# Kernel tuning notes

Measured on AMD Instinct MI355X. Metric: run time of the kernel, lower is better.

The kernel has to match this reference:

```python
import jax, jax.numpy as jnp
import numpy as np

B, N, D_IMG, D_TXT, H, C = 256, 100, 1024, 768, 512, 512
NBLK = 8
EPS = 1e-5


def setup_inputs() -> dict:
    key = jax.random.key(0)
    ks = jax.random.split(key, 24)
    rn = lambda k, s, sc=0.04: jax.random.normal(k, s, jnp.float32) * sc
    return {
        "img_embedding": jax.random.normal(ks[0], (B, D_IMG), jnp.float32),
        "func_text_embedding": jax.random.normal(ks[1], (B, D_TXT), jnp.float32),
        "node_emb": jax.random.normal(ks[2], (B, N, 768), jnp.float32),
        "pos_emb": jax.random.uniform(ks[3], (B, N, 4), jnp.float32),
        # swin head
        "swinbn_g": jnp.ones((D_IMG,)), "swinbn_b": jnp.zeros((D_IMG,)),
        "swinfc_w": rn(ks[4], (H, D_IMG)), "swinfc_b": jnp.zeros((H,)),
        # text head
        "bntext_g": jnp.ones((D_TXT,)), "bntext_b": jnp.zeros((D_TXT,)),
        "fctext_w": rn(ks[5], (H, D_TXT)), "fctext_b": jnp.zeros((H,)),
        # node / bbox heads (BatchNorm1d over channel dim = max_node)
        "bngat_g": jnp.ones((N,)), "bngat_b": jnp.zeros((N,)),
        "fcgat_w": rn(ks[6], (480, 768)), "fcgat_b": jnp.zeros((480,)),
        "bnbbox_g": jnp.ones((N,)), "bnbbox_b": jnp.zeros((N,)),
        "fcbbox_w": rn(ks[7], (32, 4), 0.3), "fcbbox_b": jnp.zeros((32,)),
        # 8 stacked Rs_GCN non-local blocks (1x1 conv weights = [out,in])
        "gcn_theta_w": rn(ks[8], (NBLK, C, C)), "gcn_theta_b": jnp.zeros((NBLK, C)),
        "gcn_phi_w": rn(ks[9], (NBLK, C, C)), "gcn_phi_b": jnp.zeros((NBLK, C)),
        "gcn_g_w": rn(ks[10], (NBLK, C, C)), "gcn_g_b": jnp.zeros((NBLK, C)),
        "gcn_W_w": rn(ks[11], (NBLK, C, C)), "gcn_W_b": jnp.zeros((NBLK, C)),
        "gcn_bn_g": jnp.ones((NBLK, C)), "gcn_bn_b": jnp.zeros((NBLK, C)),
        # final classifier
        "ffbn_g": jnp.ones((3 * H,)), "ffbn_b": jnp.zeros((3 * H,)),
        "ff_w": rn(ks[12], (2, 3 * H)), "ff_b": jnp.zeros((2,)),
    }


def _bn2(x, g, b):  # BatchNorm1d on (B, C), training-mode batch stats
    m = x.mean(0)
    v = x.var(0)
    return (x - m) * jax.lax.rsqrt(v + EPS) * g + b


def _bn_ch(x, g, b):  # BatchNorm1d on (B, C, L), channel axis 1
    m = x.mean((0, 2), keepdims=True)
    v = x.var((0, 2), keepdims=True)
    return (x - m) * jax.lax.rsqrt(v + EPS) * g[None, :, None] + b[None, :, None]


def reference(img_embedding, func_text_embedding, node_emb, pos_emb,
              swinbn_g, swinbn_b, swinfc_w, swinfc_b,
              bntext_g, bntext_b, fctext_w, fctext_b,
              bngat_g, bngat_b, fcgat_w, fcgat_b,
              bnbbox_g, bnbbox_b, fcbbox_w, fcbbox_b,
              gcn_theta_w, gcn_theta_b, gcn_phi_w, gcn_phi_b,
              gcn_g_w, gcn_g_b, gcn_W_w, gcn_W_b, gcn_bn_g, gcn_bn_b,
              ffbn_g, ffbn_b, ff_w, ff_b):
    elu = jax.nn.elu
    # image branch: x = elu(swinfc(swinbn(img)))
    x = elu(_bn2(img_embedding, swinbn_g, swinbn_b) @ swinfc_w.T + swinfc_b)
    # text branch: elu(fc_text(bn_text(text)))
    ft = elu(_bn2(func_text_embedding, bntext_g, bntext_b) @ fctext_w.T + fctext_b)
    # node / bbox branches (BN over node dim, then linear over feature dim)
    h = elu(_bn_ch(node_emb, bngat_g, bngat_b) @ fcgat_w.T + fcgat_b)       # (B,N,480)
    p = elu(_bn_ch(pos_emb, bnbbox_g, bnbbox_b) @ fcbbox_w.T + fcbbox_b)    # (B,N,32)
    v = jnp.concatenate([h, p], axis=2).transpose(0, 2, 1)                  # (B,512,N)

    # 8 non-local Rs_GCN blocks
    for i in range(NBLK):
        g_v = jnp.einsum('oc,bcn->bno', gcn_g_w[i], v) + gcn_g_b[i]          # (B,N,C)
        th_v = jnp.einsum('oc,bcn->bno', gcn_theta_w[i], v) + gcn_theta_b[i]  # (B,N,C)
        ph_v = jnp.einsum('oc,bcn->bon', gcn_phi_w[i], v) + gcn_phi_b[i][:, None]  # (B,C,N)
        R = jnp.einsum('bnc,bcm->bnm', th_v, ph_v)                            # (B,N,N)
        A = jax.nn.softmax(R, axis=-1)
        y = jnp.einsum('bnm,bmc->bcn', A, g_v)                                # (B,C,N)
        Wy = jnp.einsum('oc,bcn->bon', gcn_W_w[i], y) + gcn_W_b[i][:, None]
        Wy = _bn_ch(Wy, gcn_bn_g[i], gcn_bn_b[i])
        v = Wy + v                                                            # residual

    emb = v.transpose(0, 2, 1)  # (B,N,512)
    # l2norm normalizes over dim=1 (the node dim), matching the torch code
    emb = emb / jnp.sqrt(jnp.sum(emb * emb, axis=1, keepdims=True))
    h_feature = emb.mean(axis=1)  # (B,512)

    all_feats = jnp.concatenate([x, h_feature, ft], axis=1)  # (B,1536)
    out = _bn2(all_feats, ffbn_g, ffbn_b) @ ff_w.T + ff_b    # (B,2)
    return out
```

## Files before the change

### kernel.cpp

```cpp
#include <hip/hip_runtime.h>
#include <cstddef>

#define EPS 1e-5f

constexpr int Bsz = 256;
constexpr int Nn  = 100;
constexpr int Cc  = 512;
constexpr int BN_ROWS = Bsz * Nn;

__device__ __forceinline__ void gload_lds16(const void* g, void* l) {
    __builtin_amdgcn_global_load_lds(
        (const __attribute__((address_space(1))) void*)g,
        (__attribute__((address_space(3))) void*)l, 16, 0, 0);
}

__global__ void colstats_kernel(const float* __restrict__ x, int M, int Ccols,
                                const float* __restrict__ g, const float* __restrict__ bb,
                                float* __restrict__ s, float* __restrict__ t) {
    int c = blockIdx.x;
    int r = threadIdx.x;
    float v = (r < M) ? x[(size_t)r * Ccols + c] : 0.f;
    __shared__ float ssum[256], ssq[256];
    ssum[r] = v; ssq[r] = v * v;
    __syncthreads();
    for (int off = 128; off > 0; off >>= 1) {
        if (r < off) { ssum[r] += ssum[r + off]; ssq[r] += ssq[r + off]; }
        __syncthreads();
    }
    if (r == 0) {
        float m   = ssum[0] / M;
        float var = ssq[0] / M - m * m;
        float sc  = g[c] * rsqrtf(var + EPS);
        s[c] = sc;
        t[c] = bb[c] - m * sc;
    }
}

__global__ void chstats_kernel(const float* __restrict__ x, int D,
                               const float* __restrict__ g, const float* __restrict__ bb,
                               float* __restrict__ s, float* __restrict__ t) {
    int n = blockIdx.x;
    int tid = threadIdx.x;
    int total = Bsz * D;
    float sum = 0.f, sq = 0.f;
    for (int idx = tid; idx < total; idx += blockDim.x) {
        int b = idx / D, d = idx - b * D;
        float v = x[((size_t)b * Nn + n) * D + d];
        sum += v; sq += v * v;
    }
    __shared__ float ssum[256], ssq[256];
    ssum[tid] = sum; ssq[tid] = sq;
    __syncthreads();
    for (int off = 128; off > 0; off >>= 1) {
        if (tid < off) { ssum[tid] += ssum[tid + off]; ssq[tid] += ssq[tid + off]; }
        __syncthreads();
    }
    if (tid == 0) {
        float m   = ssum[0] / total;
        float var = ssq[0] / total - m * m;
        float sc  = g[n] * rsqrtf(var + EPS);
        s[n] = sc;
        t[n] = bb[n] - m * sc;
    }
}

__global__ void chstats_part_kernel(const float* __restrict__ x, float* __restrict__ npart) {
    int n = blockIdx.x, chunk = blockIdx.y;
    int tid = threadIdx.x;
    float sum = 0.f, sq = 0.f;
    for (int i = tid; i < 3072; i += 256) {
        int rrow = i / 192;
        int q = i - rrow * 192;
        float4 f = *(const float4*)(x + ((size_t)(chunk * 16 + rrow) * Nn + n) * 768 + q * 4);
        sum += f.x + f.y + f.z + f.w;
        sq  += f.x * f.x + f.y * f.y + f.z * f.z + f.w * f.w;
    }
    __shared__ float ss[256], s2[256];
    ss[tid] = sum; s2[tid] = sq;
    __syncthreads();
    for (int off = 128; off > 0; off >>= 1) {
        if (tid < off) { ss[tid] += ss[tid + off]; s2[tid] += s2[tid + off]; }
        __syncthreads();
    }
    if (tid == 0) {
        npart[chunk * 200 + n] = ss[0];
        npart[chunk * 200 + 100 + n] = s2[0];
    }
}

__global__ void chstats_fin_kernel(const float* __restrict__ npart,
                                   const float* __restrict__ g, const float* __restrict__ bb,
                                   float* __restrict__ s, float* __restrict__ t) {
    int n = threadIdx.x;
    if (n >= 100) return;
    float sum = 0.f, sq = 0.f;
    for (int c = 0; c < 16; c++) {
        sum += npart[c * 200 + n];
        sq  += npart[c * 200 + 100 + n];
    }
    const float total = 256.f * 768.f;
    float m   = sum / total;
    float var = sq / total - m * m;
    float sc  = g[n] * rsqrtf(var + EPS);
    s[n] = sc;
    t[n] = bb[n] - m * sc;
}

template <int NORM, bool ELU, bool TB, int KS, int BYSHIFT>
__global__ __launch_bounds__(256) void gemm128_kernel(
    const float* __restrict__ A, const float* __restrict__ B0,
    const float* __restrict__ B1, int nsplit,
    const float* __restrict__ bias,
    const float* __restrict__ s, const float* __restrict__ t,
    int M, int N, int K, int lda, int ldb, int mod,
    float* __restrict__ C, int ldc, int c_off) {
    constexpr int BS = TB ? 132 : 128;
    __shared__ float As[KS * 132];
    __shared__ float Bs[KS * BS];

    int bid = blockIdx.x;
    int xcd = bid & 7;
    int l = bid >> 3;
    int by = l & ((1 << BYSHIFT) - 1);
    int bmi = l >> BYSHIFT;
    int bm_per_xcd = (int)(gridDim.x >> (3 + BYSHIFT));
    int bm = (xcd * bm_per_xcd + bmi) * 128;

    const float* B = (by < nsplit) ? B0 : B1;
    int bn = (by < nsplit ? by : by - nsplit) * 128;
    int outcol0 = c_off + by * 128;

    int tid = threadIdx.x;
    int lane = tid & 63, wave = tid >> 6;
    int tx = tid & 15, ty = tid >> 4;

    float acc[8][8] = {};

    for (int k0 = 0; k0 < K; k0 += KS) {
#pragma unroll
        for (int i = 0; i < KS / 8; i++) {
            int id = tid + i * 256;
            int row = id / (KS / 4), q = id % (KS / 4);
            int gr = bm + row;
            float4 f = *(const float4*)(A + (size_t)gr * lda + k0 + q * 4);
            if constexpr (NORM == 2) {
                int n_ = gr % mod; float sc = s[n_], sh = t[n_];
                f.x = f.x * sc + sh; f.y = f.y * sc + sh;
                f.z = f.z * sc + sh; f.w = f.w * sc + sh;
            }
            As[(q * 4 + 0) * 132 + row] = f.x;
            As[(q * 4 + 1) * 132 + row] = f.y;
            As[(q * 4 + 2) * 132 + row] = f.z;
            As[(q * 4 + 3) * 132 + row] = f.w;
        }
        if constexpr (TB) {
#pragma unroll
            for (int i = 0; i < KS / 8; i++) {
                int id = tid + i * 256;
                int row = id / (KS / 4), q = id % (KS / 4);
                int gn = bn + row;
                float4 f = make_float4(0.f, 0.f, 0.f, 0.f);
                if (gn < N) f = *(const float4*)(B + (size_t)gn * ldb + k0 + q * 4);
                Bs[(q * 4 + 0) * BS + row] = f.x;
                Bs[(q * 4 + 1) * BS + row] = f.y;
                Bs[(q * 4 + 2) * BS + row] = f.z;
                Bs[(q * 4 + 3) * BS + row] = f.w;
            }
        } else {
#pragma unroll
            for (int i = 0; i < KS / 8; i++) {
                int r = i * 8 + wave * 2 + (lane >> 5);
                gload_lds16(B + (size_t)(k0 + r) * ldb + bn + (lane & 31) * 4,
                            (char*)&Bs[r * BS]);
            }
        }
        __syncthreads();
#pragma unroll 16
        for (int kk = 0; kk < KS; kk++) {
            float4 a0 = *(const float4*)&As[kk * 132 + ty * 4];
            float4 a1 = *(const float4*)&As[kk * 132 + ty * 4 + 64];
            float4 b0 = *(const float4*)&Bs[kk * BS + tx * 4];
            float4 b1 = *(const float4*)&Bs[kk * BS + tx * 4 + 64];
            float av[8] = {a0.x, a0.y, a0.z, a0.w, a1.x, a1.y, a1.z, a1.w};
            float bv[8] = {b0.x, b0.y, b0.z, b0.w, b1.x, b1.y, b1.z, b1.w};
#pragma unroll
            for (int i = 0; i < 8; i++)
#pragma unroll
                for (int j = 0; j < 8; j++)
                    acc[i][j] = fmaf(av[i], bv[j], acc[i][j]);
        }
        __syncthreads();
    }

#pragma unroll
    for (int i = 0; i < 8; i++) {
        int r = ty * 4 + (i & 3) + ((i & 4) ? 64 : 0);
        int gr = bm + r;
        if (gr >= M) continue;
        float* crow = C + (size_t)gr * ldc + outcol0;
#pragma unroll
        for (int h = 0; h < 2; h++) {
            int cl = tx * 4 + h * 64;
            int gcol = bn + cl;
            if constexpr (TB) { if (gcol >= N) continue; }
            float4 o;
            o.x = acc[i][h * 4 + 0]; o.y = acc[i][h * 4 + 1];
            o.z = acc[i][h * 4 + 2]; o.w = acc[i][h * 4 + 3];
            if (bias) {
                o.x += bias[gcol]; o.y += bias[gcol + 1];
                o.z += bias[gcol + 2]; o.w += bias[gcol + 3];
            }
            if constexpr (ELU) {
                o.x = o.x > 0.f ? o.x : expm1f(o.x);
                o.y = o.y > 0.f ? o.y : expm1f(o.y);
                o.z = o.z > 0.f ? o.z : expm1f(o.z);
                o.w = o.w > 0.f ? o.w : expm1f(o.w);
            }
            *(float4*)(crow + cl) = o;
        }
    }
}

template <int NORM, bool ELU, bool TB>
__global__ void gemm_kernel(const float* __restrict__ A, const float* __restrict__ B,
                            const float* __restrict__ bias,
                            const float* __restrict__ s, const float* __restrict__ t,
                            int M, int N, int K, int lda, int ldb, int mod,
                            float* __restrict__ Cout, int ldc, int c_off) {
    __shared__ float As[16][65];
    __shared__ float Bs[16][65];

    int bm = blockIdx.x * 64, bn = blockIdx.y * 64;
    int tid = threadIdx.x;
    int tm = (tid >> 4) << 2;
    int tn = (tid & 15) << 2;
    float acc[4][4] = {};

    for (int k0 = 0; k0 < K; k0 += 16) {
#pragma unroll
        for (int i = 0; i < 4; i++) {
            int idx = tid + i * 256;
            {
                int rr = idx >> 4, kk = idx & 15;
                int gr = bm + rr, gk = k0 + kk;
                float av = 0.f;
                if (gr < M && gk < K) {
                    av = A[(size_t)gr * lda + gk];
                    if constexpr (NORM == 1) av = av * s[gk] + t[gk];
                    else if constexpr (NORM == 2) { int n_ = gr % mod; av = av * s[n_] + t[n_]; }
                }
                As[kk][rr] = av;
            }
            if constexpr (TB) {
                int nn = idx >> 4, kk = idx & 15;
                int gn = bn + nn, gk = k0 + kk;
                Bs[kk][nn] = (gn < N && gk < K) ? B[(size_t)gn * ldb + gk] : 0.f;
            } else {
                int kk = idx >> 6, nn = idx & 63;
                int gn = bn + nn, gk = k0 + kk;
                Bs[kk][nn] = (gn < N && gk < K) ? B[(size_t)gk * ldb + gn] : 0.f;
            }
        }
        __syncthreads();
#pragma unroll
        for (int kk = 0; kk < 16; kk++) {
            float a0[4], b0[4];
#pragma unroll
            for (int i = 0; i < 4; i++) a0[i] = As[kk][tm + i];
#pragma unroll
            for (int j = 0; j < 4; j++) b0[j] = Bs[kk][tn + j];
#pragma unroll
            for (int i = 0; i < 4; i++)
#pragma unroll
                for (int j = 0; j < 4; j++)
                    acc[i][j] = fmaf(a0[i], b0[j], acc[i][j]);
        }
        __syncthreads();
    }

#pragma unroll
    for (int i = 0; i < 4; i++) {
        int gr = bm + tm + i;
        if (gr >= M) continue;
#pragma unroll
        for (int j = 0; j < 4; j++) {
            int gn = bn + tn + j;
            if (gn >= N) continue;
            float v = acc[i][j] + (bias ? bias[gn] : 0.f);
            if constexpr (ELU) v = v > 0.f ? v : expm1f(v);
            Cout[(size_t)gr * ldc + c_off + gn] = v;
        }
    }
}

__global__ __launch_bounds__(256) void compose_kernel(
    const float* __restrict__ th, const float* __restrict__ ph,
    const float* __restrict__ g, const float* __restrict__ W,
    float* __restrict__ Mw, float* __restrict__ WGT) {
    __shared__ float As[32][33];
    __shared__ float Bs[32][68];
    int z = blockIdx.z;
    const float* A = z ? g : th;
    int bm = blockIdx.x * 32, bn = blockIdx.y * 64;
    int tid = threadIdx.x;
    int tm = (tid >> 4) * 2, tn = (tid & 15) * 4;
    float acc[2][4] = {};

    for (int k0 = 0; k0 < Cc; k0 += 32) {
#pragma unroll
        for (int i = 0; i < 4; i++) {
            int id = tid + i * 256;
            int kk = id >> 5, m = id & 31;
            As[kk][m] = A[(size_t)(k0 + kk) * Cc + bm + m];
        }
#pragma unroll
        for (int i = 0; i < 8; i++) {
            int id = tid + i * 256;
            if (z == 0) {
                int kk = id >> 6, n = id & 63;
                Bs[kk][n] = ph[(size_t)(k0 + kk) * Cc + bn + n];
            } else {
                int n = id >> 5, kk = id & 31;
                Bs[kk][n] = W[(size_t)(bn + n) * Cc + k0 + kk];
            }
        }
        __syncthreads();
#pragma unroll
        for (int kk = 0; kk < 32; kk++) {
            float a0 = As[kk][tm], a1 = As[kk][tm + 1];
            float4 b4 = *(const float4*)&Bs[kk][tn];
            acc[0][0] = fmaf(a0, b4.x, acc[0][0]);
            acc[0][1] = fmaf(a0, b4.y, acc[0][1]);
            acc[0][2] = fmaf(a0, b4.z, acc[0][2]);
            acc[0][3] = fmaf(a0, b4.w, acc[0][3]);
            acc[1][0] = fmaf(a1, b4.x, acc[1][0]);
            acc[1][1] = fmaf(a1, b4.y, acc[1][1]);
            acc[1][2] = fmaf(a1, b4.z, acc[1][2]);
            acc[1][3] = fmaf(a1, b4.w, acc[1][3]);
        }
        __syncthreads();
    }
    float* out = z ? WGT : Mw;
    *(float4*)&out[(size_t)(bm + tm) * Cc + bn + tn] =
        make_float4(acc[0][0], acc[0][1], acc[0][2], acc[0][3]);
    *(float4*)&out[(size_t)(bm + tm + 1) * Cc + bn + tn] =
        make_float4(acc[1][0], acc[1][1], acc[1][2], acc[1][3]);
}

__global__ void bbox_kernel(const float* __restrict__ pos, const float* __restrict__ w,
                            const float* __restrict__ bias, const float* __restrict__ s,
                            const float* __restrict__ t, float* __restrict__ V) {
    __shared__ float ws[32][4];
    int tid = threadIdx.x;
    if (tid < 128) ws[tid >> 2][tid & 3] = w[tid];
    __syncthreads();
    int r = blockIdx.x * 8 + (tid >> 5);
    int o = tid & 31;
    int n = r % Nn;
    float sc = s[n], sh = t[n];
    float p0 = pos[(size_t)r * 4 + 0] * sc + sh;
    float p1 = pos[(size_t)r * 4 + 1] * sc + sh;
    float p2 = pos[(size_t)r * 4 + 2] * sc + sh;
    float p3 = pos[(size_t)r * 4 + 3] * sc + sh;
    float acc = bias[o] + p0 * ws[o][0] + p1 * ws[o][1] + p2 * ws[o][2] + p3 * ws[o][3];
    acc = acc > 0.f ? acc : expm1f(acc);
    V[(size_t)r * Cc + 480 + o] = acc;
}

__global__ void q2_kernel(const float* __restrict__ phi, const float* __restrict__ thb,
                          float* __restrict__ q2) {
    int c = blockIdx.x;
    int l = threadIdx.x;
    float acc = 0.f;
    for (int j = l; j < Cc; j += 64) acc += phi[(size_t)j * Cc + c] * thb[j];
    for (int off = 32; off > 0; off >>= 1) acc += __shfl_xor(acc, off, 64);
    if (l == 0) q2[c] = acc;
}
__global__ void cconst_kernel(const float* __restrict__ W, const float* __restrict__ gb,
                              const float* __restrict__ Wb, float* __restrict__ cc) {
    int o = blockIdx.x;
    int l = threadIdx.x;
    float acc = 0.f;
    for (int j = l; j < Cc; j += 64) acc += W[(size_t)o * Cc + j] * gb[j];
    for (int off = 32; off > 0; off >>= 1) acc += __shfl_xor(acc, off, 64);
    if (l == 0) cc[o] = acc + Wb[o];
}

__global__ __launch_bounds__(256) void attn_rs_kernel(
    const float* __restrict__ TZ, const float* __restrict__ V,
    const float* __restrict__ q2, float* __restrict__ Abuf) {
    __shared__ float smem[5500];
    float* Ts = smem;
    float* Vs = smem + 1800;
    float* A_lds = smem;
    float* ct_lds = smem + 5400;

    int bid = blockIdx.x;
    int xcd = bid & 7;
    int l = bid >> 3;
    int b = xcd * 32 + (l >> 1);
    int rh = l & 1;
    int row0 = b * Nn + rh * 50;
    int tid = threadIdx.x;
    int tx = tid & 31, ty = tid >> 5;

    {
        int r = tid >> 1, h = tid & 1;
        float cacc = 0.f;
        if (r < Nn) {
            const float4* vp = (const float4*)(V + (size_t)(b * Nn + r) * 512);
            const float4* qp = (const float4*)q2;
            for (int c4 = h; c4 < 128; c4 += 2) {
                float4 f = vp[c4], q = qp[c4];
                cacc += f.x * q.x + f.y * q.y + f.z * q.z + f.w * q.w;
            }
        }
        cacc += __shfl_xor(cacc, 1, 64);
        if (r < Nn && h == 0) ct_lds[r] = cacc;
    }

    float acc[7][4];
#pragma unroll
    for (int i = 0; i < 7; i++)
#pragma unroll
        for (int j = 0; j < 4; j++) acc[i][j] = 0.f;

    for (int kt = 0; kt < 16; kt++) {
        __syncthreads();
        for (int i = tid; i < 1200; i += 256) {
            if (i < 400) {
                int r = i >> 3, q = i & 7;
                float4 f = *(const float4*)(TZ + (size_t)(row0 + r) * 1024 + kt * 32 + q * 4);
                *(float4*)&Ts[r * 36 + q * 4] = f;
            } else {
                int ii = i - 400;
                int r = ii >> 3, q = ii & 7;
                float4 f = *(const float4*)(V + (size_t)(b * Nn + r) * 512 + kt * 32 + q * 4);
                *(float4*)&Vs[r * 36 + q * 4] = f;
            }
        }
        __syncthreads();
#pragma unroll
        for (int q = 0; q < 8; q++) {
            float4 av[7];
#pragma unroll
            for (int i = 0; i < 7; i++)
                av[i] = *(const float4*)&Ts[(ty * 7 + i) * 36 + q * 4];
            float4 bv[4];
#pragma unroll
            for (int j = 0; j < 4; j++)
                bv[j] = *(const float4*)&Vs[(tx + 32 * j) * 36 + q * 4];
#pragma unroll
            for (int kk = 0; kk < 4; kk++) {
#pragma unroll
                for (int i = 0; i < 7; i++) {
                    float a = ((const float*)&av[i])[kk];
#pragma unroll
                    for (int j = 0; j < 4; j++)
                        acc[i][j] = fmaf(a, ((const float*)&bv[j])[kk], acc[i][j]);
                }
            }
        }
    }
    __syncthreads();

    float ctv[4];
#pragma unroll
    for (int j = 0; j < 4; j++) {
        int c = tx + 32 * j;
        ctv[j] = (c < Nn) ? ct_lds[c] : 0.f;
    }
#pragma unroll
    for (int i = 0; i < 7; i++) {
        int r = ty * 7 + i;
        if (r >= 50) continue;
#pragma unroll
        for (int j = 0; j < 4; j++) {
            int c = tx + 32 * j;
            if (c < Nn) A_lds[r * 105 + c] = acc[i][j] + ctv[j];
        }
    }
    __syncthreads();
    if (tid < 50) {
        float* row = A_lds + tid * 105;
        float mx = -1e30f;
        for (int m = 0; m < Nn; m++) mx = fmaxf(mx, row[m]);
        float sm = 0.f;
        for (int m = 0; m < Nn; m++) { float e = expf(row[m] - mx); row[m] = e; sm += e; }
        float inv = 1.f / sm;
        for (int m = 0; m < Nn; m++) row[m] *= inv;
    }
    __syncthreads();
    for (int i = tid; i < 5000; i += 256) {
        int r = i / 100, c = i - r * 100;
        Abuf[(size_t)(row0 + r) * 104 + c] = A_lds[r * 105 + c];
    }
}

__global__ __launch_bounds__(256) void pv_kernel(
    float* __restrict__ TZ, const float* __restrict__ Abuf,
    const float* __restrict__ cc, float* __restrict__ part) {
    __shared__ float Zs[25 * 256];
    __shared__ float As2[50 * 28];
    int bid = blockIdx.x;
    int xcd = bid & 7;
    int l = bid >> 3;
    int b = xcd * 32 + (l >> 2);
    int sub = l & 3;
    int rh = sub & 1;
    int ch = sub >> 1;
    int row0 = b * Nn + rh * 50;
    int tid = threadIdx.x;
    int lane = tid & 63, wave = tid >> 6;
    int tx = tid & 31, ty = tid >> 5;

    float acc[7][8];
#pragma unroll
    for (int i = 0; i < 7; i++)
#pragma unroll
        for (int j = 0; j < 8; j++) acc[i][j] = 0.f;

    for (int kt = 0; kt < 4; kt++) {
        __syncthreads();
        for (int r = wave; r < 25; r += 4) {
            gload_lds16(TZ + (size_t)(b * Nn + kt * 25 + r) * 1024 + 512 + ch * 256 + lane * 4,
                        (char*)&Zs[r * 256]);
        }
        for (int i = tid; i < 1250; i += 256) {
            int r = i / 25, k = i - r * 25;
            As2[r * 28 + k] = Abuf[(size_t)(row0 + r) * 104 + kt * 25 + k];
        }
        __syncthreads();
#pragma unroll 5
        for (int k = 0; k < 25; k++) {
            float av[7];
#pragma unroll
            for (int i = 0; i < 7; i++) av[i] = As2[(ty * 7 + i) * 28 + k];
            float zv[8];
#pragma unroll
            for (int j = 0; j < 8; j++) zv[j] = Zs[k * 256 + tx + 32 * j];
#pragma unroll
            for (int i = 0; i < 7; i++)
#pragma unroll
                for (int j = 0; j < 8; j++)
                    acc[i][j] = fmaf(av[i], zv[j], acc[i][j]);
        }
    }

    float ccv[8];
#pragma unroll
    for (int j = 0; j < 8; j++) ccv[j] = cc[ch * 256 + tx + 32 * j];
    float psum[8], psq[8];
#pragma unroll
    for (int j = 0; j < 8; j++) { psum[j] = 0.f; psq[j] = 0.f; }
#pragma unroll
    for (int i = 0; i < 7; i++) {
        int r = ty * 7 + i;
        if (r >= 50) continue;
        float* orow = TZ + (size_t)(row0 + r) * 1024 + ch * 256;
#pragma unroll
        for (int j = 0; j < 8; j++) {
            float v = acc[i][j] + ccv[j];
            orow[tx + 32 * j] = v;
            psum[j] += v; psq[j] += v * v;
        }
    }
    __syncthreads();
    float* sums = Zs;
#pragma unroll
    for (int j = 0; j < 8; j++) {
        int c = tx + 32 * j;
        sums[ty * 512 + c] = psum[j];
        sums[ty * 512 + 256 + c] = psq[j];
    }
    __syncthreads();
    {
        float ssv = 0.f, sqv = 0.f;
        for (int y = 0; y < 8; y++) {
            ssv += sums[y * 512 + tid];
            sqv += sums[y * 512 + 256 + tid];
        }
        int pair = b * 2 + rh;
        part[(size_t)pair * 1024 + ch * 256 + tid] = ssv;
        part[(size_t)pair * 1024 + 512 + ch * 256 + tid] = sqv;
    }
}

__global__ void wy_fin2_kernel(const float* __restrict__ part,
                               const float* __restrict__ g, const float* __restrict__ bb,
                               float* __restrict__ s, float* __restrict__ t) {
    int c = blockIdx.x;
    int l = threadIdx.x;
    float sum = 0.f, sq = 0.f;
    for (int p = l; p < 512; p += 64) {
        sum += part[(size_t)p * 1024 + c];
        sq  += part[(size_t)p * 1024 + 512 + c];
    }
    for (int off = 32; off > 0; off >>= 1) {
        sum += __shfl_xor(sum, off, 64);
        sq  += __shfl_xor(sq, off, 64);
    }
    if (l == 0) {
        float m   = sum / BN_ROWS;
        float var = sq / BN_ROWS - m * m;
        float sc  = g[c] * rsqrtf(var + EPS);
        s[c] = sc;
        t[c] = bb[c] - m * sc;
    }
}

__global__ void residual_kernel(float* __restrict__ V, const float* __restrict__ Wy, int ldw,
                                const float* __restrict__ s, const float* __restrict__ t) {
    size_t total4 = (size_t)BN_ROWS * Cc / 4;
    for (size_t i4 = (size_t)blockIdx.x * blockDim.x + threadIdx.x; i4 < total4;
         i4 += (size_t)gridDim.x * blockDim.x) {
        int row = (int)(i4 >> 7);
        int c = (int)(i4 & 127) * 4;
        float4 w = *(const float4*)(Wy + (size_t)row * ldw + c);
        float4 sv = *(const float4*)(s + c);
        float4 tv = *(const float4*)(t + c);
        float4 v = *(float4*)(V + (size_t)row * Cc + c);
        v.x += w.x * sv.x + tv.x; v.y += w.y * sv.y + tv.y;
        v.z += w.z * sv.z + tv.z; v.w += w.w * sv.w + tv.w;
        *(float4*)(V + (size_t)row * Cc + c) = v;
    }
}

__global__ void l2norm_mean_kernel(const float* __restrict__ V, float* __restrict__ ALL) {
    int b = blockIdx.x;
    int c = threadIdx.x;
    float sum = 0.f, sq = 0.f;
    const float* p = V + (size_t)b * Nn * Cc + c;
    for (int n = 0; n < Nn; n++) {
        float v = p[(size_t)n * Cc];
        sum += v; sq += v * v;
    }
    ALL[(size_t)b * 1536 + 512 + c] = sum / (Nn * sqrtf(sq));
}

__global__ void final_kernel(const float* __restrict__ ALL, const float* __restrict__ s,
                             const float* __restrict__ t, const float* __restrict__ w,
                             const float* __restrict__ bias, float* __restrict__ out) {
    int b = blockIdx.x;
    int tid = threadIdx.x;
    float p0 = 0.f, p1 = 0.f;
    for (int k = tid; k < 1536; k += 256) {
        float af = ALL[(size_t)b * 1536 + k] * s[k] + t[k];
        p0 += af * w[k];
        p1 += af * w[1536 + k];
    }
    __shared__ float s0[256], s1[256];
    s0[tid] = p0; s1[tid] = p1;
    __syncthreads();
    for (int off = 128; off > 0; off >>= 1) {
        if (tid < off) { s0[tid] += s0[tid + off]; s1[tid] += s1[tid + off]; }
        __syncthreads();
    }
    if (tid == 0) {
        out[b * 2 + 0] = s0[0] + bias[0];
        out[b * 2 + 1] = s1[0] + bias[1];
    }
}

extern "C" void kernel_launch(void* const* d_in, const int* in_sizes, int n_in,
                              void* d_out, int out_size, void* d_ws, size_t ws_size,
                              hipStream_t stream) {
    const float* img   = (const float*)d_in[0];
    const float* txt   = (const float*)d_in[1];
    const float* node  = (const float*)d_in[2];
    const float* pos   = (const float*)d_in[3];
    const float* swinbn_g = (const float*)d_in[4];
    const float* swinbn_b = (const float*)d_in[5];
    const float* swinfc_w = (const float*)d_in[6];
    const float* swinfc_b = (const float*)d_in[7];
    const float* bntext_g = (const float*)d_in[8];
    const float* bntext_b = (const float*)d_in[9];
    const float* fctext_w = (const float*)d_in[10];
    const float* fctext_b = (const float*)d_in[11];
    const float* bngat_g  = (const float*)d_in[12];
    const float* bngat_b  = (const float*)d_in[13];
    const float* fcgat_w  = (const float*)d_in[14];
    const float* fcgat_b  = (const float*)d_in[15];
    const float* bnbbox_g = (const float*)d_in[16];
    const float* bnbbox_b = (const float*)d_in[17];
    const float* fcbbox_w = (const float*)d_in[18];
    const float* fcbbox_b = (const float*)d_in[19];
    const float* gcn_theta_w = (const float*)d_in[20];
    const float* gcn_theta_b = (const float*)d_in[21];
    const float* gcn_phi_w   = (const float*)d_in[22];
    const float* gcn_phi_b   = (const float*)d_in[23];
    const float* gcn_g_w     = (const float*)d_in[24];
    const float* gcn_g_b     = (const float*)d_in[25];
    const float* gcn_W_w     = (const float*)d_in[26];
    const float* gcn_W_b     = (const float*)d_in[27];
    const float* gcn_bn_g    = (const float*)d_in[28];
    const float* gcn_bn_b    = (const float*)d_in[29];
    const float* ffbn_g = (const float*)d_in[30];
    const float* ffbn_b = (const float*)d_in[31];
    const float* ff_w   = (const float*)d_in[32];
    const float* ff_b   = (const float*)d_in[33];

    float* ws = (float*)d_ws;
    const size_t VN = (size_t)BN_ROWS * Cc;
    float* V    = ws;
    float* TZ   = V + VN;
    float* Abuf = TZ + VN * 2;
    float* Mw   = Abuf + (size_t)BN_ROWS * 104;
    float* WGT  = Mw + (size_t)Cc * Cc;
    float* ALL  = WGT + (size_t)Cc * Cc;
    float* part = ALL + (size_t)Bsz * 1536;
    float* st   = part + 524288;
    float* s_img = st;            float* t_img = s_img + 1024;
    float* s_txt = t_img + 1024;  float* t_txt = s_txt + 768;
    float* s_nd  = t_txt + 768;   float* t_nd  = s_nd + 128;
    float* s_bb  = t_nd + 128;    float* t_bb  = s_bb + 128;
    float* s_g   = t_bb + 128;    float* t_g   = s_g + 512;
    float* s_ff  = t_g + 512;     float* t_ff  = s_ff + 1536;
    float* q2    = t_ff + 1536;   float* cc    = q2 + 512;

    dim3 blk(256);

    colstats_kernel<<<1024, 256, 0, stream>>>(img, 256, 1024, swinbn_g, swinbn_b, s_img, t_img);
    colstats_kernel<<<768, 256, 0, stream>>>(txt, 256, 768, bntext_g, bntext_b, s_txt, t_txt);
    chstats_part_kernel<<<dim3(100, 16, 1), 256, 0, stream>>>(node, part);
    chstats_fin_kernel<<<1, 128, 0, stream>>>(part, bngat_g, bngat_b, s_nd, t_nd);
    chstats_kernel<<<100, 256, 0, stream>>>(pos, 4, bnbbox_g, bnbbox_b, s_bb, t_bb);

    gemm_kernel<1, true, true><<<dim3(4, 8, 1), blk, 0, stream>>>(
        img, swinfc_w, swinfc_b, s_img, t_img, 256, 512, 1024, 1024, 1024, 0,
        ALL, 1536, 0);
    gemm_kernel<1, true, true><<<dim3(4, 8, 1), blk, 0, stream>>>(
        txt, fctext_w, fctext_b, s_txt, t_txt, 256, 512, 768, 768, 768, 0,
        ALL, 1536, 1024);
    gemm128_kernel<2, true, true, 32, 2><<<800, blk, 0, stream>>>(
        node, fcgat_w, nullptr, 1 << 30, fcgat_b, s_nd, t_nd,
        25600, 480, 768, 768, 768, 100, V, 512, 0);
    bbox_kernel<<<3200, 256, 0, stream>>>(pos, fcbbox_w, fcbbox_b, s_bb, t_bb, V);

    for (int i = 0; i < 8; i++) {
        const float* thw = gcn_theta_w + (size_t)i * Cc * Cc;
        const float* thb = gcn_theta_b + (size_t)i * Cc;
        const float* phw = gcn_phi_w + (size_t)i * Cc * Cc;
        const float* gw  = gcn_g_w + (size_t)i * Cc * Cc;
        const float* gb  = gcn_g_b + (size_t)i * Cc;
        const float* Ww  = gcn_W_w + (size_t)i * Cc * Cc;
        const float* Wb  = gcn_W_b + (size_t)i * Cc;

        compose_kernel<<<dim3(16, 8, 2), blk, 0, stream>>>(thw, phw, gw, Ww, Mw, WGT);
        q2_kernel<<<512, 64, 0, stream>>>(phw, thb, q2);
        cconst_kernel<<<512, 64, 0, stream>>>(Ww, gb, Wb, cc);

        gemm128_kernel<0, false, false, 32, 3><<<1600, blk, 0, stream>>>(
            V, Mw, WGT, 4, nullptr, nullptr, nullptr,
            25600, 1024, 512, 512, 512, 0, TZ, 1024, 0);

        attn_rs_kernel<<<512, blk, 0, stream>>>(TZ, V, q2, Abuf);
        pv_kernel<<<1024, blk, 0, stream>>>(TZ, Abuf, cc, part);

        wy_fin2_kernel<<<512, 64, 0, stream>>>(part, gcn_bn_g + (size_t)i * Cc,
                                               gcn_bn_b + (size_t)i * Cc, s_g, t_g);
        residual_kernel<<<2048, 256, 0, stream>>>(V, TZ, 1024, s_g, t_g);
    }

    l2norm_mean_kernel<<<256, 512, 0, stream>>>(V, ALL);
    colstats_kernel<<<1536, 256, 0, stream>>>(ALL, 256, 1536, ffbn_g, ffbn_b, s_ff, t_ff);
    final_kernel<<<256, 256, 0, stream>>>(ALL, s_ff, t_ff, ff_w, ff_b, (float*)d_out);
}
```

Before: 5.204 ms.

## Fuse attention softmax with PV stage and batch per-block weight precomputation

Merges the attention-score/softmax kernel with the A·Z product kernel so the softmax matrix stays in LDS instead of round-tripping through a global Abuf. All eight blocks' composed weight matrices and bias vectors are now computed up front in single batched launches rather than three small launches per block. The fcgat weight is pre-transposed and padded to 512 columns so the node GEMM uses the non-transposed B path. The fused kernel launches half as many blocks (512 vs 1024) and uses about 47KB of LDS, which lowers parallelism and occupancy for the PV part.

```diff
diff --git a/kernel.cpp b/kernel.cpp
--- a/kernel.cpp
+++ b/kernel.cpp
@@ -104,6 +104,28 @@
     float sc  = g[n] * rsqrtf(var + EPS);
     s[n] = sc;
     t[n] = bb[n] - m * sc;
+}
+
+__global__ void transpose_w_kernel(const float* __restrict__ w, const float* __restrict__ bias,
+                                   float* __restrict__ WT, float* __restrict__ pb) {
+    __shared__ float tile[32][33];
+    int kb = blockIdx.x * 32, nb = blockIdx.y * 32;
+    int tx = threadIdx.x & 31, ty = threadIdx.x >> 5;
+#pragma unroll
+    for (int i = 0; i < 4; i++) {
+        int n = nb + ty + i * 8;
+        tile[ty + i * 8][tx] = (n < 480) ? w[(size_t)n * 768 + kb + tx] : 0.f;
+    }
+    __syncthreads();
+#pragma unroll
+    for (int i = 0; i < 4; i++) {
+        int k = kb + ty + i * 8;
+        WT[(size_t)k * 512 + nb + tx] = tile[tx][ty + i * 8];
+    }
+    if (blockIdx.x == 0 && threadIdx.x < 32) {
+        int n = nb + threadIdx.x;
+        pb[n] = (n < 480) ? bias[n] : 0.f;
+    }
 }
 
 template <int NORM, bool ELU, bool TB, int KS, int BYSHIFT>
@@ -294,13 +316,17 @@
 }
 
 __global__ __launch_bounds__(256) void compose_kernel(
-    const float* __restrict__ th, const float* __restrict__ ph,
-    const float* __restrict__ g, const float* __restrict__ W,
-    float* __restrict__ Mw, float* __restrict__ WGT) {
+    const float* __restrict__ thw, const float* __restrict__ phw,
+    const float* __restrict__ gw, const float* __restrict__ Ww,
+    float* __restrict__ Mw_all, float* __restrict__ WGT_all) {
     __shared__ float As[32][33];
     __shared__ float Bs[32][68];
-    int z = blockIdx.z;
-    const float* A = z ? g : th;
+    int blk = blockIdx.z >> 1;
+    int z = blockIdx.z & 1;
+    size_t woff = (size_t)blk * Cc * Cc;
+    const float* A = (z ? gw : thw) + woff;
+    const float* ph = phw + woff;
+    const float* W = Ww + woff;
     int bm = blockIdx.x * 32, bn = blockIdx.y * 64;
     int tid = threadIdx.x;
     int tm = (tid >> 4) * 2, tn = (tid & 15) * 4;
@@ -340,11 +366,35 @@
         }
         __syncthreads();
     }
-    float* out = z ? WGT : Mw;
+    float* out = (z ? WGT_all : Mw_all) + woff;
     *(float4*)&out[(size_t)(bm + tm) * Cc + bn + tn] =
         make_float4(acc[0][0], acc[0][1], acc[0][2], acc[0][3]);
     *(float4*)&out[(size_t)(bm + tm + 1) * Cc + bn + tn] =
         make_float4(acc[1][0], acc[1][1], acc[1][2], acc[1][3]);
+}
+
+__global__ void qc_kernel(const float* __restrict__ phw, const float* __restrict__ thb,
+                          const float* __restrict__ Ww, const float* __restrict__ gb,
+                          const float* __restrict__ Wb,
+                          float* __restrict__ q2a, float* __restrict__ cca) {
+    int blk = blockIdx.y >> 1;
+    int type = blockIdx.y & 1;
+    int c = blockIdx.x;
+    int l = threadIdx.x;
+    float acc = 0.f;
+    if (type == 0) {
+        const float* phi = phw + (size_t)blk * Cc * Cc;
+        const float* tb = thb + (size_t)blk * Cc;
+        for (int j = l; j < Cc; j += 64) acc += phi[(size_t)j * Cc + c] * tb[j];
+        for (int off = 32; off > 0; off >>= 1) acc += __shfl_xor(acc, off, 64);
+        if (l == 0) q2a[blk * Cc + c] = acc;
+    } else {
+        const float* W = Ww + (size_t)blk * Cc * Cc;
+        const float* gbb = gb + (size_t)blk * Cc;
+        for (int j = l; j < Cc; j += 64) acc += W[(size_t)c * Cc + j] * gbb[j];
+        for (int off = 32; off > 0; off >>= 1) acc += __shfl_xor(acc, off, 64);
+        if (l == 0) cca[blk * Cc + c] = acc + Wb[(size_t)blk * Cc + c];
+    }
 }
 
 __global__ void bbox_kernel(const float* __restrict__ pos, const float* __restrict__ w,
@@ -367,33 +417,16 @@
     V[(size_t)r * Cc + 480 + o] = acc;
 }
 
-__global__ void q2_kernel(const float* __restrict__ phi, const float* __restrict__ thb,
-                          float* __restrict__ q2) {
-    int c = blockIdx.x;
-    int l = threadIdx.x;
-    float acc = 0.f;
-    for (int j = l; j < Cc; j += 64) acc += phi[(size_t)j * Cc + c] * thb[j];
-    for (int off = 32; off > 0; off >>= 1) acc += __shfl_xor(acc, off, 64);
-    if (l == 0) q2[c] = acc;
-}
-__global__ void cconst_kernel(const float* __restrict__ W, const float* __restrict__ gb,
-                              const float* __restrict__ Wb, float* __restrict__ cc) {
-    int o = blockIdx.x;
-    int l = threadIdx.x;
-    float acc = 0.f;
-    for (int j = l; j < Cc; j += 64) acc += W[(size_t)o * Cc + j] * gb[j];
-    for (int off = 32; off > 0; off >>= 1) acc += __shfl_xor(acc, off, 64);
-    if (l == 0) cc[o] = acc + Wb[o];
-}
-
-__global__ __launch_bounds__(256) void attn_rs_kernel(
-    const float* __restrict__ TZ, const float* __restrict__ V,
-    const float* __restrict__ q2, float* __restrict__ Abuf) {
-    __shared__ float smem[5500];
+__global__ __launch_bounds__(256) void attn_fused_kernel(
+    float* __restrict__ TZ, const float* __restrict__ V,
+    const float* __restrict__ q2, const float* __restrict__ cc,
+    float* __restrict__ part) {
+    __shared__ float smem[11904];
     float* Ts = smem;
     float* Vs = smem + 1800;
     float* A_lds = smem;
     float* ct_lds = smem + 5400;
+    float* Zs = smem + 5504;
 
     int bid = blockIdx.x;
     int xcd = bid & 7;
@@ -402,6 +435,7 @@
     int rh = l & 1;
     int row0 = b * Nn + rh * 50;
     int tid = threadIdx.x;
+    int lane = tid & 63, wave = tid >> 6;
     int tx = tid & 31, ty = tid >> 5;
 
     {
@@ -490,99 +524,75 @@
         float inv = 1.f / sm;
         for (int m = 0; m < Nn; m++) row[m] *= inv;
     }
-    __syncthreads();
-    for (int i = tid; i < 5000; i += 256) {
-        int r = i / 100, c = i - r * 100;
-        Abuf[(size_t)(row0 + r) * 104 + c] = A_lds[r * 105 + c];
-    }
-}
-
-__global__ __launch_bounds__(256) void pv_kernel(
-    float* __restrict__ TZ, const float* __restrict__ Abuf,
-    const float* __restrict__ cc, float* __restrict__ part) {
-    __shared__ float Zs[25 * 256];
-    __shared__ float As2[50 * 28];
-    int bid = blockIdx.x;
-    int xcd = bid & 7;
-    int l = bid >> 3;
-    int b = xcd * 32 + (l >> 2);
-    int sub = l & 3;
-    int rh = sub & 1;
-    int ch = sub >> 1;
-    int row0 = b * Nn + rh * 50;
-    int tid = threadIdx.x;
-    int lane = tid & 63, wave = tid >> 6;
-    int tx = tid & 31, ty = tid >> 5;
-
-    float acc[7][8];
-#pragma unroll
-    for (int i = 0; i < 7; i++)
-#pragma unroll
-        for (int j = 0; j < 8; j++) acc[i][j] = 0.f;
-
-    for (int kt = 0; kt < 4; kt++) {
-        __syncthreads();
-        for (int r = wave; r < 25; r += 4) {
-            gload_lds16(TZ + (size_t)(b * Nn + kt * 25 + r) * 1024 + 512 + ch * 256 + lane * 4,
-                        (char*)&Zs[r * 256]);
-        }
-        for (int i = tid; i < 1250; i += 256) {
-            int r = i / 25, k = i - r * 25;
-            As2[r * 28 + k] = Abuf[(size_t)(row0 + r) * 104 + kt * 25 + k];
-        }
-        __syncthreads();
+
+    int pair = b * 2 + rh;
+    for (int ch = 0; ch < 2; ch++) {
+        float acc2[7][8];
+#pragma unroll
+        for (int i = 0; i < 7; i++)
+#pragma unroll
+            for (int j = 0; j < 8; j++) acc2[i][j] = 0.f;
+
+        for (int kt = 0; kt < 4; kt++) {
+            __syncthreads();
+            for (int r = wave; r < 25; r += 4) {
+                gload_lds16(TZ + (size_t)(b * Nn + kt * 25 + r) * 1024 + 512 + ch * 256 + lane * 4,
+                            (char*)&Zs[r * 256]);
+            }
+            __syncthreads();
 #pragma unroll 5
-        for (int k = 0; k < 25; k++) {
-            float av[7];
-#pragma unroll
-            for (int i = 0; i < 7; i++) av[i] = As2[(ty * 7 + i) * 28 + k];
-            float zv[8];
-#pragma unroll
-            for (int j = 0; j < 8; j++) zv[j] = Zs[k * 256 + tx + 32 * j];
-#pragma unroll
-            for (int i = 0; i < 7; i++)
-#pragma unroll
-                for (int j = 0; j < 8; j++)
-                    acc[i][j] = fmaf(av[i], zv[j], acc[i][j]);
-        }
-    }
-
-    float ccv[8];
-#pragma unroll
-    for (int j = 0; j < 8; j++) ccv[j] = cc[ch * 256 + tx + 32 * j];
-    float psum[8], psq[8];
-#pragma unroll
-    for (int j = 0; j < 8; j++) { psum[j] = 0.f; psq[j] = 0.f; }
-#pragma unroll
-    for (int i = 0; i < 7; i++) {
-        int r = ty * 7 + i;
-        if (r >= 50) continue;
-        float* orow = TZ + (size_t)(row0 + r) * 1024 + ch * 256;
+            for (int k2 = 0; k2 < 25; k2++) {
+                int k = kt * 25 + k2;
+                float av[7];
+#pragma unroll
+                for (int i = 0; i < 7; i++) av[i] = A_lds[(ty * 7 + i) * 105 + k];
+                float zv[8];
+#pragma unroll
+                for (int j = 0; j < 8; j++) zv[j] = Zs[k2 * 256 + tx + 32 * j];
+#pragma unroll
+                for (int i = 0; i < 7; i++)
+#pragma unroll
+                    for (int j = 0; j < 8; j++)
+                        acc2[i][j] = fmaf(av[i], zv[j], acc2[i][j]);
+            }
+        }
+
+        float ccv[8];
+#pragma unroll
+        for (int j = 0; j < 8; j++) ccv[j] = cc[ch * 256 + tx + 32 * j];
+        float psum[8], psq[8];
+#pragma unroll
+        for (int j = 0; j < 8; j++) { psum[j] = 0.f; psq[j] = 0.f; }
+#pragma unroll
+        for (int i = 0; i < 7; i++) {
+            int r = ty * 7 + i;
+            if (r >= 50) continue;
+            float* orow = TZ + (size_t)(row0 + r) * 1024 + ch * 256;
+#pragma unroll
+            for (int j = 0; j < 8; j++) {
+                float v = acc2[i][j] + ccv[j];
+                orow[tx + 32 * j] = v;
+                psum[j] += v; psq[j] += v * v;
+            }
+        }
+        __syncthreads();
+        float* sums = Zs;
 #pragma unroll
         for (int j = 0; j < 8; j++) {
-            float v = acc[i][j] + ccv[j];
-            orow[tx + 32 * j] = v;
-            psum[j] += v; psq[j] += v * v;
-        }
-    }
-    __syncthreads();
-    float* sums = Zs;
-#pragma unroll
-    for (int j = 0; j < 8; j++) {
-        int c = tx + 32 * j;
-        sums[ty * 512 + c] = psum[j];
-        sums[ty * 512 + 256 + c] = psq[j];
-    }
-    __syncthreads();
-    {
-        float ssv = 0.f, sqv = 0.f;
-        for (int y = 0; y < 8; y++) {
-            ssv += sums[y * 512 + tid];
-            sqv += sums[y * 512 + 256 + tid];
-        }
-        int pair = b * 2 + rh;
-        part[(size_t)pair * 1024 + ch * 256 + tid] = ssv;
-        part[(size_t)pair * 1024 + 512 + ch * 256 + tid] = sqv;
+            int c = tx + 32 * j;
+            sums[ty * 512 + c] = psum[j];
+            sums[ty * 512 + 256 + c] = psq[j];
+        }
+        __syncthreads();
+        {
+            float ssv = 0.f, sqv = 0.f;
+            for (int y = 0; y < 8; y++) {
+                ssv += sums[y * 512 + tid];
+                sqv += sums[y * 512 + 256 + tid];
+            }
+            part[(size_t)pair * 1024 + ch * 256 + tid] = ssv;
+            part[(size_t)pair * 1024 + 512 + ch * 256 + tid] = sqv;
+        }
     }
 }
 
@@ -702,21 +712,24 @@
 
     float* ws = (float*)d_ws;
     const size_t VN = (size_t)BN_ROWS * Cc;
-    float* V    = ws;
-    float* TZ   = V + VN;
-    float* Abuf = TZ + VN * 2;
-    float* Mw   = Abuf + (size_t)BN_ROWS * 104;
-    float* WGT  = Mw + (size_t)Cc * Cc;
-    float* ALL  = WGT + (size_t)Cc * Cc;
-    float* part = ALL + (size_t)Bsz * 1536;
-    float* st   = part + 524288;
+    const size_t CC2 = (size_t)Cc * Cc;
+    float* V       = ws;
+    float* TZ      = V + VN;
+    float* Mw_all  = TZ + VN * 2;
+    float* WGT_all = Mw_all + 8 * CC2;
+    float* WT      = WGT_all + 8 * CC2;
+    float* ALL     = WT + 393216;
+    float* part    = ALL + (size_t)Bsz * 1536;
+    float* q2_all  = part + 524288;
+    float* cc_all  = q2_all + 4096;
+    float* st      = cc_all + 4096;
     float* s_img = st;            float* t_img = s_img + 1024;
     float* s_txt = t_img + 1024;  float* t_txt = s_txt + 768;
     float* s_nd  = t_txt + 768;   float* t_nd  = s_nd + 128;
     float* s_bb  = t_nd + 128;    float* t_bb  = s_bb + 128;
     float* s_g   = t_bb + 128;    float* t_g   = s_g + 512;
     float* s_ff  = t_g + 512;     float* t_ff  = s_ff + 1536;
-    float* q2    = t_ff + 1536;   float* cc    = q2 + 512;
+    float* pb    = t_ff + 1536;
 
     dim3 blk(256);
 
@@ -732,30 +745,25 @@
     gemm_kernel<1, true, true><<<dim3(4, 8, 1), blk, 0, stream>>>(
         txt, fctext_w, fctext_b, s_txt, t_txt, 256, 512, 768, 768, 768, 0,
         ALL, 1536, 1024);
-    gemm128_kernel<2, true, true, 32, 2><<<800, blk, 0, stream>>>(
-        node, fcgat_w, nullptr, 1 << 30, fcgat_b, s_nd, t_nd,
-        25600, 480, 768, 768, 768, 100, V, 512, 0);
+    transpose_w_kernel<<<dim3(24, 16, 1), blk, 0, stream>>>(fcgat_w, fcgat_b, WT, pb);
+    gemm128_kernel<2, true, false, 32, 2><<<800, blk, 0, stream>>>(
+        node, WT, nullptr, 4, pb, s_nd, t_nd,
+        25600, 512, 768, 768, 512, 100, V, 512, 0);
     bbox_kernel<<<3200, 256, 0, stream>>>(pos, fcbbox_w, fcbbox_b, s_bb, t_bb, V);
 
+    compose_kernel<<<dim3(16, 8, 16), blk, 0, stream>>>(
+        gcn_theta_w, gcn_phi_w, gcn_g_w, gcn_W_w, Mw_all, WGT_all);
+    qc_kernel<<<dim3(512, 16, 1), 64, 0, stream>>>(
+        gcn_phi_w, gcn_theta_b, gcn_W_w, gcn_g_b, gcn_W_b, q2_all, cc_all);
+
     for (int i = 0; i < 8; i++) {
-        const float* thw = gcn_theta_w + (size_t)i * Cc * Cc;
-        const float* thb = gcn_theta_b + (size_t)i * Cc;
-        const float* phw = gcn_phi_w + (size_t)i * Cc * Cc;
-        const float* gw  = gcn_g_w + (size_t)i * Cc * Cc;
-        const float* gb  = gcn_g_b + (size_t)i * Cc;
-        const float* Ww  = gcn_W_w + (size_t)i * Cc * Cc;
-        const float* Wb  = gcn_W_b + (size_t)i * Cc;
-
-        compose_kernel<<<dim3(16, 8, 2), blk, 0, stream>>>(thw, phw, gw, Ww, Mw, WGT);
-        q2_kernel<<<512, 64, 0, stream>>>(phw, thb, q2);
-        cconst_kernel<<<512, 64, 0, stream>>>(Ww, gb, Wb, cc);
-
         gemm128_kernel<0, false, false, 32, 3><<<1600, blk, 0, stream>>>(
-            V, Mw, WGT, 4, nullptr, nullptr, nullptr,
+            V, Mw_all + (size_t)i * CC2, WGT_all + (size_t)i * CC2, 4,
+            nullptr, nullptr, nullptr,
             25600, 1024, 512, 512, 512, 0, TZ, 1024, 0);
 
-        attn_rs_kernel<<<512, blk, 0, stream>>>(TZ, V, q2, Abuf);
-        pv_kernel<<<1024, blk, 0, stream>>>(TZ, Abuf, cc, part);
+        attn_fused_kernel<<<512, blk, 0, stream>>>(
+            TZ, V, q2_all + (size_t)i * Cc, cc_all + (size_t)i * Cc, part);
 
         wy_fin2_kernel<<<512, 64, 0, stream>>>(part, gcn_bn_g + (size_t)i * Cc,
                                                gcn_bn_b + (size_t)i * Cc, s_g, t_g);
```

New measurement: 4.678 ms. 10.1% less time.
